# Kernel tuning notes

Hardware: AMD Instinct MI355X
Metric: run time of the kernel (lower is better)

The kernel has to match this reference:

```python
import jax, jax.numpy as jnp
import numpy as np

N_NODES = 100000
N_EDGES = 400000
N_GRAPHS = 4096
F_IN, HID, HEADS, OUT_DIM = 64, 64, 4, 128
NEG_SLOPE = 0.2


def gat_layer(x, src, dst, W, a_s, a_d, b, concat):
    # x: [N, Fin]; W: [Fin, H*C]; a_s/a_d: [H, C]; src/dst: [Etot] (self loops included)
    N = x.shape[0]
    H, C = a_s.shape
    h = (x @ W).reshape(N, H, C)
    e_src = jnp.einsum('nhc,hc->nh', h, a_s)  # [N, H]
    e_dst = jnp.einsum('nhc,hc->nh', h, a_d)
    e = jax.nn.leaky_relu(e_src[src] + e_dst[dst], NEG_SLOPE)  # [Etot, H]
    # segment softmax over edges grouped by destination node
    m = jax.ops.segment_max(e, dst, num_segments=N)
    m = jnp.where(jnp.isfinite(m), m, 0.0)
    ex = jnp.exp(e - m[dst])
    denom = jax.ops.segment_sum(ex, dst, num_segments=N)
    alpha = ex / jnp.maximum(denom[dst], 1e-16)  # [Etot, H]
    out = jax.ops.segment_sum(alpha[:, :, None] * h[src], dst, num_segments=N)  # [N, H, C]
    out = out.reshape(N, H * C) if concat else out.mean(axis=1)
    return out + b


def setup_inputs() -> dict:
    key = jax.random.key(0)
    ks = jax.random.split(key, 32)
    x = jax.random.normal(ks[0], (N_NODES, F_IN), dtype=jnp.float32)
    edge_index = jax.random.randint(ks[1], (2, N_EDGES), 0, N_NODES, dtype=jnp.int64) if jax.config.jax_enable_x64 else jax.random.randint(ks[1], (2, N_EDGES), 0, N_NODES).astype(jnp.int32)
    batch = jnp.sort(jax.random.randint(ks[2], (N_NODES,), 0, N_GRAPHS)).astype(edge_index.dtype)
    s = 0.1
    d = {
        'x': x, 'edge_index': edge_index, 'batch': batch, 'num_graphs': N_GRAPHS,
        'W0': jax.random.normal(ks[3], (F_IN, HEADS * HID), jnp.float32) * s,
        'as0': jax.random.normal(ks[4], (HEADS, HID), jnp.float32) * s,
        'ad0': jax.random.normal(ks[5], (HEADS, HID), jnp.float32) * s,
        'b0': jnp.zeros((HEADS * HID,), jnp.float32),
        'W1': jax.random.normal(ks[6], (HEADS * HID, HEADS * HID), jnp.float32) * s,
        'as1': jax.random.normal(ks[7], (HEADS, HID), jnp.float32) * s,
        'ad1': jax.random.normal(ks[8], (HEADS, HID), jnp.float32) * s,
        'b1': jnp.zeros((HEADS * HID,), jnp.float32),
        'W2': jax.random.normal(ks[9], (HEADS * HID, HEADS * HID), jnp.float32) * s,
        'as2': jax.random.normal(ks[10], (HEADS, HID), jnp.float32) * s,
        'ad2': jax.random.normal(ks[11], (HEADS, HID), jnp.float32) * s,
        'b2': jnp.zeros((HEADS * HID,), jnp.float32),
        'W3': jax.random.normal(ks[12], (HEADS * HID, OUT_DIM), jnp.float32) * s,
        'as3': jax.random.normal(ks[13], (1, OUT_DIM), jnp.float32) * s,
        'ad3': jax.random.normal(ks[14], (1, OUT_DIM), jnp.float32) * s,
        'b3': jnp.zeros((OUT_DIM,), jnp.float32),
        'mW0': jax.random.normal(ks[15], (OUT_DIM, OUT_DIM // 2), jnp.float32) * s,
        'mb0': jnp.zeros((OUT_DIM // 2,), jnp.float32),
        'mW1': jax.random.normal(ks[16], (OUT_DIM // 2, OUT_DIM // 4), jnp.float32) * s,
        'mb1': jnp.zeros((OUT_DIM // 4,), jnp.float32),
        'mW2': jax.random.normal(ks[17], (OUT_DIM // 4, 4), jnp.float32) * s,
        'mb2': jnp.zeros((4,), jnp.float32),
    }
    return d


def reference(x, edge_index, batch, num_graphs, W0, as0, ad0, b0, W1, as1, ad1, b1,
              W2, as2, ad2, b2, W3, as3, ad3, b3, mW0, mb0, mW1, mb1, mW2, mb2):
    N = x.shape[0]
    # PyG GATConv default add_self_loops=True
    loop = jnp.arange(N, dtype=edge_index.dtype)
    src = jnp.concatenate([edge_index[0], loop])
    dst = jnp.concatenate([edge_index[1], loop])
    # dropout layers are identity in eval mode
    h = gat_layer(x, src, dst, W0, as0, ad0, b0, concat=True)
    h = jax.nn.elu(h)
    h = gat_layer(h, src, dst, W1, as1, ad1, b1, concat=True)
    h = jax.nn.elu(h)
    h = gat_layer(h, src, dst, W2, as2, ad2, b2, concat=True)
    h = jax.nn.elu(h)
    h = gat_layer(h, src, dst, W3, as3, ad3, b3, concat=False)  # [N, OUT_DIM]
    # global mean pool per graph
    sums = jax.ops.segment_sum(h, batch, num_segments=num_graphs)
    cnt = jax.ops.segment_sum(jnp.ones((N,), h.dtype), batch, num_segments=num_graphs)
    pooled = sums / jnp.maximum(cnt, 1.0)[:, None]  # [G, OUT_DIM]
    # MLPReadout(out_dim, 4, L=2): 128 -> 64 -> 32 -> 4 with ReLU between
    y = jax.nn.relu(pooled @ mW0 + mb0)
    y = jax.nn.relu(y @ mW1 + mb1)
    y = y @ mW2 + mb2
    return y
```

## Files before the change

kernel.cpp:

```cpp
#include <hip/hip_runtime.h>
#include <math.h>

#define N_NODES 100000
#define N_EDGES 400000
#define N_GRAPHS_C 4096
#define E_TOT (N_EDGES + N_NODES)

static inline int ceil_div(int a, int b) { return (a + b - 1) / b; }

typedef __attribute__((ext_vector_type(8))) short short8v;
typedef __attribute__((ext_vector_type(4))) float float4v;

__device__ __forceinline__ float b2f(unsigned short u) {
  union { unsigned int i; float f; } v;
  v.i = ((unsigned int)u) << 16;
  return v.f;
}
__device__ __forceinline__ unsigned short f2b(float f) {
  union { float f; unsigned int i; } v;
  v.f = f;
  unsigned int x = v.i;
  unsigned int r = x + 0x7fffu + ((x >> 16) & 1u);
  return (unsigned short)(r >> 16);
}


__global__ __launch_bounds__(256) void k_cvt_x(const float* __restrict__ in, unsigned short* __restrict__ out,
                                               int n4) {
  int i = blockIdx.x * 256 + threadIdx.x;
  if (i >= n4) return;
  float4 v = *(const float4*)(in + (size_t)i * 4);
  ushort4 o;
  o.x = f2b(v.x); o.y = f2b(v.y); o.z = f2b(v.z); o.w = f2b(v.w);
  *(ushort4*)(out + (size_t)i * 4) = o;
}

__global__ __launch_bounds__(256) void k_cvt_wt(const float* __restrict__ W, unsigned short* __restrict__ Wt,
                                                int K, int Ncol) {
  int i = blockIdx.x * 256 + threadIdx.x;
  if (i >= K * Ncol) return;
  int n = i / K, k = i % K;
  Wt[(size_t)n * K + k] = f2b(W[(size_t)k * Ncol + n]);
}


__global__ __launch_bounds__(256) void k_count_deg(const int* __restrict__ ei, int* __restrict__ deg) {
  int i = blockIdx.x * 256 + threadIdx.x;
  if (i < N_EDGES) atomicAdd(&deg[ei[N_EDGES + i]], 1);
}

__global__ __launch_bounds__(256) void k_scan(int* __restrict__ deg, int* __restrict__ offs,
                                              int* __restrict__ cursor, int* __restrict__ counter) {
  __shared__ int sm[256];
  __shared__ int sbase;
  int tid = threadIdx.x;
  int n = blockIdx.x * 256 + tid;
  int d = (n < N_NODES) ? (deg[n] + 1) : 0;
  sm[tid] = d;
  __syncthreads();
  for (int off = 1; off < 256; off <<= 1) {
    int v = (tid >= off) ? sm[tid - off] : 0;
    __syncthreads();
    sm[tid] += v;
    __syncthreads();
  }
  if (tid == 255) sbase = atomicAdd(counter, sm[255]);
  __syncthreads();
  int excl = sm[tid] - d;
  if (n < N_NODES) {
    int o = sbase + excl;
    offs[n] = o;
    cursor[n] = o;
    deg[n] = d;
  }
}

__global__ __launch_bounds__(256) void k_scatter(const int* __restrict__ ei, int* __restrict__ cursor,
                                                 int* __restrict__ csr, int* __restrict__ csr_dst) {
  int i = blockIdx.x * 256 + threadIdx.x;
  if (i < N_EDGES) {
    int d = ei[N_EDGES + i];
    int pos = atomicAdd(&cursor[d], 1);
    csr[pos] = ei[i];
    csr_dst[pos] = d;
  } else if (i < E_TOT) {
    int n = i - N_EDGES;
    int pos = atomicAdd(&cursor[n], 1);
    csr[pos] = n;
    csr_dst[pos] = n;
  }
}


__global__ __launch_bounds__(256) void k_gcount(const int* __restrict__ batch, int* __restrict__ gcnt) {
  int i = blockIdx.x * 256 + threadIdx.x;
  if (i < N_NODES) atomicAdd(&gcnt[batch[i]], 1);
}

__global__ __launch_bounds__(256) void k_gscan(const int* __restrict__ gcnt, int* __restrict__ gptr) {
  __shared__ int sm[256];
  __shared__ int srun;
  int tid = threadIdx.x;
  if (tid == 0) srun = 0;
  __syncthreads();
  for (int c = 0; c < N_GRAPHS_C / 256; c++) {
    int idx = c * 256 + tid;
    int v = gcnt[idx];
    sm[tid] = v;
    __syncthreads();
    for (int off = 1; off < 256; off <<= 1) {
      int t = (tid >= off) ? sm[tid - off] : 0;
      __syncthreads();
      sm[tid] += t;
      __syncthreads();
    }
    gptr[idx] = srun + sm[tid] - v;
    __syncthreads();
    if (tid == 0) srun += sm[255];
    __syncthreads();
  }
}


#define LDA 40

template <int ATT>
__global__ __launch_bounds__(256) void k_gemm_bf16(const unsigned short* __restrict__ A,
                                                   const unsigned short* __restrict__ Wt,
                                                   unsigned short* __restrict__ out, int M, int K, int Ncol,
                                                   const float* __restrict__ a_s, const float* __restrict__ a_d,
                                                   float* __restrict__ es, float* __restrict__ ed) {
  __shared__ unsigned short As[128 * LDA];
  __shared__ unsigned short Bs[128 * LDA];
  int tid = threadIdx.x;
  int wave = tid >> 6, lane = tid & 63;
  int quad = lane >> 4, l16 = lane & 15;
  int wrow = (wave & 1) * 64, wcol = (wave >> 1) * 64;
  int row0 = blockIdx.x * 128, col0 = blockIdx.y * 128;

  float4v acc[4][4];
#pragma unroll
  for (int i = 0; i < 4; i++)
#pragma unroll
    for (int j = 0; j < 4; j++) acc[i][j] = (float4v)(0.f);

  int r0 = tid >> 2, c0 = (tid & 3) * 8;
  int r1 = (tid + 256) >> 2, c1 = c0;

  for (int k0 = 0; k0 < K; k0 += 32) {
    uint4 a0 = make_uint4(0, 0, 0, 0), a1 = make_uint4(0, 0, 0, 0);
    if (row0 + r0 < M) a0 = *(const uint4*)(A + (size_t)(row0 + r0) * K + k0 + c0);
    if (row0 + r1 < M) a1 = *(const uint4*)(A + (size_t)(row0 + r1) * K + k0 + c1);
    uint4 b0 = *(const uint4*)(Wt + (size_t)(col0 + r0) * K + k0 + c0);
    uint4 b1 = *(const uint4*)(Wt + (size_t)(col0 + r1) * K + k0 + c1);
    __syncthreads();
    *(uint4*)(&As[r0 * LDA + c0]) = a0;
    *(uint4*)(&As[r1 * LDA + c1]) = a1;
    *(uint4*)(&Bs[r0 * LDA + c0]) = b0;
    *(uint4*)(&Bs[r1 * LDA + c1]) = b1;
    __syncthreads();

    short8v af[4], bf[4];
#pragma unroll
    for (int i = 0; i < 4; i++)
      af[i] = *(const short8v*)(&As[(wrow + i * 16 + l16) * LDA + quad * 8]);
#pragma unroll
    for (int j = 0; j < 4; j++)
      bf[j] = *(const short8v*)(&Bs[(wcol + j * 16 + l16) * LDA + quad * 8]);
#pragma unroll
    for (int i = 0; i < 4; i++)
#pragma unroll
      for (int j = 0; j < 4; j++)
        acc[i][j] = __builtin_amdgcn_mfma_f32_16x16x32_bf16(af[i], bf[j], acc[i][j], 0, 0, 0);
  }

#pragma unroll
  for (int i = 0; i < 4; i++) {
#pragma unroll
    for (int r = 0; r < 4; r++) {
      int m = row0 + wrow + i * 16 + quad * 4 + r;
      if (m < M) {
#pragma unroll
        for (int j = 0; j < 4; j++) {
          int col = col0 + wcol + j * 16 + l16;
          out[(size_t)m * Ncol + col] = f2b(acc[i][j][r]);
        }
      }
    }
  }

  if (ATT) {
    int h = (col0 + wcol) >> 6;
    float as_r[4], ad_r[4];
#pragma unroll
    for (int j = 0; j < 4; j++) {
      as_r[j] = a_s[h * 64 + j * 16 + l16];
      ad_r[j] = a_d[h * 64 + j * 16 + l16];
    }
#pragma unroll
    for (int i = 0; i < 4; i++) {
#pragma unroll
      for (int r = 0; r < 4; r++) {
        float pes = acc[i][0][r] * as_r[0] + acc[i][1][r] * as_r[1] + acc[i][2][r] * as_r[2] + acc[i][3][r] * as_r[3];
        float ped = acc[i][0][r] * ad_r[0] + acc[i][1][r] * ad_r[1] + acc[i][2][r] * ad_r[2] + acc[i][3][r] * ad_r[3];
#pragma unroll
        for (int mk = 1; mk < 16; mk <<= 1) {
          pes += __shfl_xor(pes, mk, 64);
          ped += __shfl_xor(ped, mk, 64);
        }
        if (l16 == 0) {
          int m = row0 + wrow + i * 16 + quad * 4 + r;
          if (m < M) {
            es[m * 4 + h] = pes;
            ed[m * 4 + h] = ped;
          }
        }
      }
    }
  }
}


template <int H, int C>
__global__ __launch_bounds__(256) void k_att(const unsigned short* __restrict__ hbuf,
                                             const float* __restrict__ a_s, const float* __restrict__ a_d,
                                             float* __restrict__ es, float* __restrict__ ed) {
  int idx = blockIdx.x * 256 + threadIdx.x;
  if (idx >= N_NODES * H) return;
  int n = idx / H;
  int h = idx % H;
  const unsigned short* row = hbuf + (size_t)n * (H * C) + h * C;
  const float* asp = a_s + h * C;
  const float* adp = a_d + h * C;
  float s = 0.f, d = 0.f;
#pragma unroll
  for (int c = 0; c < C; c += 8) {
    uint4 u = *(const uint4*)(row + c);
    float4 s0 = *(const float4*)(asp + c);
    float4 s1 = *(const float4*)(asp + c + 4);
    float4 d0 = *(const float4*)(adp + c);
    float4 d1 = *(const float4*)(adp + c + 4);
    float v0 = b2f((unsigned short)(u.x & 0xffff)), v1 = b2f((unsigned short)(u.x >> 16));
    float v2 = b2f((unsigned short)(u.y & 0xffff)), v3 = b2f((unsigned short)(u.y >> 16));
    float v4 = b2f((unsigned short)(u.z & 0xffff)), v5 = b2f((unsigned short)(u.z >> 16));
    float v6 = b2f((unsigned short)(u.w & 0xffff)), v7 = b2f((unsigned short)(u.w >> 16));
    s += v0 * s0.x + v1 * s0.y + v2 * s0.z + v3 * s0.w + v4 * s1.x + v5 * s1.y + v6 * s1.z + v7 * s1.w;
    d += v0 * d0.x + v1 * d0.y + v2 * d0.z + v3 * d0.w + v4 * d1.x + v5 * d1.y + v6 * d1.z + v7 * d1.w;
  }
  es[idx] = s;
  ed[idx] = d;
}


template <int H>
__global__ __launch_bounds__(256) void k_edge_logits(const float* __restrict__ es, const float* __restrict__ ed,
                                                     const int* __restrict__ csr, const int* __restrict__ csr_dst,
                                                     float* __restrict__ ew) {
  int p = blockIdx.x * 256 + threadIdx.x;
  if (p >= E_TOT) return;
  int s = csr[p], d = csr_dst[p];
  if (H == 4) {
    float4 a = *(const float4*)(es + (size_t)s * 4);
    float4 b = *(const float4*)(ed + (size_t)d * 4);
    float4 e;
    e.x = a.x + b.x; e.x = e.x > 0.f ? e.x : 0.2f * e.x;
    e.y = a.y + b.y; e.y = e.y > 0.f ? e.y : 0.2f * e.y;
    e.z = a.z + b.z; e.z = e.z > 0.f ? e.z : 0.2f * e.z;
    e.w = a.w + b.w; e.w = e.w > 0.f ? e.w : 0.2f * e.w;
    *(float4*)(ew + (size_t)p * 4) = e;
  } else {
    float e = es[s] + ed[d];
    ew[p] = e > 0.f ? e : 0.2f * e;
  }
}


template <int H>
__global__ __launch_bounds__(256) void k_stats(float* __restrict__ ew, const int* __restrict__ offs,
                                               const int* __restrict__ deg) {
  int idx = blockIdx.x * 256 + threadIdx.x;
  if (idx >= N_NODES * H) return;
  int n = (H == 1) ? idx : (idx >> 2);
  int h = (H == 1) ? 0 : (idx & 3);
  float* p = ew + (size_t)offs[n] * H + h;
  int c = deg[n];
  float m = -1e30f;
  for (int i = 0; i < c; i++) m = fmaxf(m, p[(size_t)i * H]);
  float s = 0.f;
  for (int i = 0; i < c; i++) s += __expf(p[(size_t)i * H] - m);
  float inv = 1.0f / fmaxf(s, 1e-16f);
  for (int i = 0; i < c; i++) p[(size_t)i * H] = __expf(p[(size_t)i * H] - m) * inv;
}


__device__ __forceinline__ void acc4(float* acc, float w, uint2 u) {
  acc[0] += w * b2f((unsigned short)(u.x & 0xffff));
  acc[1] += w * b2f((unsigned short)(u.x >> 16));
  acc[2] += w * b2f((unsigned short)(u.y & 0xffff));
  acc[3] += w * b2f((unsigned short)(u.y >> 16));
}
__device__ __forceinline__ void acc2(float* acc, float w, unsigned int u) {
  acc[0] += w * b2f((unsigned short)(u & 0xffff));
  acc[1] += w * b2f((unsigned short)(u >> 16));
}

template <int H, int C>
__global__ __launch_bounds__(256) void k_aggregate(const unsigned short* __restrict__ hbuf,
                                                   const float* __restrict__ ew,
                                                   const int* __restrict__ offs, const int* __restrict__ deg,
                                                   const int* __restrict__ csr, const float* __restrict__ bias,
                                                   unsigned short* __restrict__ out, int applyElu) {
  constexpr int F = H * C;
  constexpr int VPL = F / 64;
  int wave = threadIdx.x >> 6;
  int lane = threadIdx.x & 63;
  int n = blockIdx.x * 4 + wave;
  if (n >= N_NODES) return;
  int head = (H == 1) ? 0 : (lane >> 4);
  int start = offs[n];
  int cnt = deg[n];
  const float* ewp = ew + (size_t)start * H + head;
  const int* csrp = csr + start;

  float acc[VPL];
#pragma unroll
  for (int j = 0; j < VPL; j++) acc[j] = 0.f;

  int i = 0;
  for (; i + 4 <= cnt; i += 4) {
    int s0 = csrp[i], s1 = csrp[i + 1], s2 = csrp[i + 2], s3 = csrp[i + 3];
    float w0 = ewp[(size_t)(i + 0) * H];
    float w1 = ewp[(size_t)(i + 1) * H];
    float w2 = ewp[(size_t)(i + 2) * H];
    float w3 = ewp[(size_t)(i + 3) * H];
    if (VPL == 4) {
      uint2 u0 = *(const uint2*)(hbuf + (size_t)s0 * F + lane * 4);
      uint2 u1 = *(const uint2*)(hbuf + (size_t)s1 * F + lane * 4);
      uint2 u2 = *(const uint2*)(hbuf + (size_t)s2 * F + lane * 4);
      uint2 u3 = *(const uint2*)(hbuf + (size_t)s3 * F + lane * 4);
      acc4(acc, w0, u0); acc4(acc, w1, u1); acc4(acc, w2, u2); acc4(acc, w3, u3);
    } else {
      unsigned int u0 = *(const unsigned int*)(hbuf + (size_t)s0 * F + lane * 2);
      unsigned int u1 = *(const unsigned int*)(hbuf + (size_t)s1 * F + lane * 2);
      unsigned int u2 = *(const unsigned int*)(hbuf + (size_t)s2 * F + lane * 2);
      unsigned int u3 = *(const unsigned int*)(hbuf + (size_t)s3 * F + lane * 2);
      acc2(acc, w0, u0); acc2(acc, w1, u1); acc2(acc, w2, u2); acc2(acc, w3, u3);
    }
  }
  for (; i < cnt; i++) {
    int s = csrp[i];
    float w = ewp[(size_t)i * H];
    if (VPL == 4) {
      uint2 u = *(const uint2*)(hbuf + (size_t)s * F + lane * 4);
      acc4(acc, w, u);
    } else {
      unsigned int u = *(const unsigned int*)(hbuf + (size_t)s * F + lane * 2);
      acc2(acc, w, u);
    }
  }

  unsigned short ob[VPL];
#pragma unroll
  for (int j = 0; j < VPL; j++) {
    float v = acc[j] + bias[lane * VPL + j];
    if (applyElu) v = v > 0.f ? v : expm1f(v);
    ob[j] = f2b(v);
  }
  if (VPL == 4) {
    ushort4 o = make_ushort4(ob[0], ob[1], ob[2], ob[3]);
    *(ushort4*)(out + (size_t)n * F + lane * 4) = o;
  } else {
    ushort2 o = make_ushort2(ob[0], ob[1]);
    *(ushort2*)(out + (size_t)n * F + lane * 2) = o;
  }
}


__global__ __launch_bounds__(256) void k_pool_seg(const unsigned short* __restrict__ feat,
                                                  const int* __restrict__ gptr, const int* __restrict__ gcnt,
                                                  float* __restrict__ pool) {
  int wave = threadIdx.x >> 6;
  int lane = threadIdx.x & 63;
  int g = blockIdx.x * 4 + wave;
  if (g >= N_GRAPHS_C) return;
  int start = gptr[g];
  int c = gcnt[g];
  float a0 = 0.f, a1 = 0.f;
  int i = 0;
  for (; i + 2 <= c; i += 2) {
    unsigned int u0 = *(const unsigned int*)(feat + (size_t)(start + i) * 128 + lane * 2);
    unsigned int u1 = *(const unsigned int*)(feat + (size_t)(start + i + 1) * 128 + lane * 2);
    a0 += b2f((unsigned short)(u0 & 0xffff)) + b2f((unsigned short)(u1 & 0xffff));
    a1 += b2f((unsigned short)(u0 >> 16)) + b2f((unsigned short)(u1 >> 16));
  }
  if (i < c) {
    unsigned int u = *(const unsigned int*)(feat + (size_t)(start + i) * 128 + lane * 2);
    a0 += b2f((unsigned short)(u & 0xffff));
    a1 += b2f((unsigned short)(u >> 16));
  }
  float invc = 1.0f / fmaxf((float)c, 1.0f);
  pool[(size_t)g * 128 + lane * 2 + 0] = a0 * invc;
  pool[(size_t)g * 128 + lane * 2 + 1] = a1 * invc;
}


__global__ __launch_bounds__(128) void k_readout(const float* __restrict__ pool,
                                                 const float* __restrict__ mW0, const float* __restrict__ mb0,
                                                 const float* __restrict__ mW1, const float* __restrict__ mb1,
                                                 const float* __restrict__ mW2, const float* __restrict__ mb2,
                                                 float* __restrict__ out) {
  __shared__ float p[128];
  __shared__ float y1[64];
  __shared__ float y2[32];
  int g = blockIdx.x;
  int t = threadIdx.x;
  p[t] = pool[(size_t)g * 128 + t];
  __syncthreads();
  if (t < 64) {
    float a = mb0[t];
#pragma unroll 4
    for (int k = 0; k < 128; k++) a += p[k] * mW0[k * 64 + t];
    y1[t] = a > 0.f ? a : 0.f;
  }
  __syncthreads();
  if (t < 32) {
    float a = mb1[t];
#pragma unroll 4
    for (int k = 0; k < 64; k++) a += y1[k] * mW1[k * 32 + t];
    y2[t] = a > 0.f ? a : 0.f;
  }
  __syncthreads();
  if (t < 4) {
    float a = mb2[t];
#pragma unroll 4
    for (int k = 0; k < 32; k++) a += y2[k] * mW2[k * 4 + t];
    out[(size_t)g * 4 + t] = a;
  }
}


extern "C" void kernel_launch(void* const* d_in, const int* in_sizes, int n_in,
                              void* d_out, int out_size, void* d_ws, size_t ws_size,
                              hipStream_t stream) {
  const float* x = (const float*)d_in[0];
  const int* ei = (const int*)d_in[1];
  const int* batch = (const int*)d_in[2];
  const float* W0 = (const float*)d_in[4];
  const float* as0 = (const float*)d_in[5];
  const float* ad0 = (const float*)d_in[6];
  const float* b0 = (const float*)d_in[7];
  const float* W1 = (const float*)d_in[8];
  const float* as1 = (const float*)d_in[9];
  const float* ad1 = (const float*)d_in[10];
  const float* b1 = (const float*)d_in[11];
  const float* W2 = (const float*)d_in[12];
  const float* as2 = (const float*)d_in[13];
  const float* ad2 = (const float*)d_in[14];
  const float* b2 = (const float*)d_in[15];
  const float* W3 = (const float*)d_in[16];
  const float* as3 = (const float*)d_in[17];
  const float* ad3 = (const float*)d_in[18];
  const float* b3 = (const float*)d_in[19];
  const float* mW0 = (const float*)d_in[20];
  const float* mb0 = (const float*)d_in[21];
  const float* mW1 = (const float*)d_in[22];
  const float* mb1 = (const float*)d_in[23];
  const float* mW2 = (const float*)d_in[24];
  const float* mb2 = (const float*)d_in[25];
  float* out = (float*)d_out;

  char* ws = (char*)d_ws;
  size_t cur = 0;
  auto alloc = [&](size_t bytes) -> char* {
    char* p = ws + cur;
    cur += (bytes + 255) & ~(size_t)255;
    return p;
  };
  unsigned short* featA = (unsigned short*)alloc((size_t)N_NODES * 256 * 2);
  unsigned short* hB = (unsigned short*)alloc((size_t)N_NODES * 256 * 2);
  unsigned short* xb = (unsigned short*)alloc((size_t)N_NODES * 64 * 2);
  unsigned short* wt0 = (unsigned short*)alloc((size_t)256 * 64 * 2);
  unsigned short* wt1 = (unsigned short*)alloc((size_t)256 * 256 * 2);
  unsigned short* wt2 = (unsigned short*)alloc((size_t)256 * 256 * 2);
  unsigned short* wt3 = (unsigned short*)alloc((size_t)128 * 256 * 2);
  float* es = (float*)alloc((size_t)N_NODES * 4 * sizeof(float));
  float* ed = (float*)alloc((size_t)N_NODES * 4 * sizeof(float));
  float* ew = (float*)alloc((size_t)E_TOT * 4 * sizeof(float));
  int* deg = (int*)alloc((size_t)N_NODES * sizeof(int));
  int* offs = (int*)alloc((size_t)N_NODES * sizeof(int));
  int* cursor = (int*)alloc((size_t)N_NODES * sizeof(int));
  int* csr = (int*)alloc((size_t)E_TOT * sizeof(int));
  int* csr_dst = (int*)alloc((size_t)E_TOT * sizeof(int));
  float* pool = (float*)alloc((size_t)N_GRAPHS_C * 128 * sizeof(float));
  int* gcnt = (int*)alloc((size_t)N_GRAPHS_C * sizeof(int));
  int* gptr = (int*)alloc((size_t)N_GRAPHS_C * sizeof(int));
  int* counter = (int*)alloc(256);
  (void)ws_size; (void)in_sizes; (void)n_in; (void)out_size;

  k_cvt_x<<<ceil_div(N_NODES * 64 / 4, 256), 256, 0, stream>>>(x, xb, N_NODES * 64 / 4);
  k_cvt_wt<<<ceil_div(64 * 256, 256), 256, 0, stream>>>(W0, wt0, 64, 256);
  k_cvt_wt<<<ceil_div(256 * 256, 256), 256, 0, stream>>>(W1, wt1, 256, 256);
  k_cvt_wt<<<ceil_div(256 * 256, 256), 256, 0, stream>>>(W2, wt2, 256, 256);
  k_cvt_wt<<<ceil_div(256 * 128, 256), 256, 0, stream>>>(W3, wt3, 256, 128);

  hipMemsetAsync(deg, 0, (size_t)N_NODES * sizeof(int), stream);
  hipMemsetAsync(counter, 0, sizeof(int), stream);
  hipMemsetAsync(gcnt, 0, (size_t)N_GRAPHS_C * sizeof(int), stream);
  k_count_deg<<<ceil_div(N_EDGES, 256), 256, 0, stream>>>(ei, deg);
  k_scan<<<ceil_div(N_NODES, 256), 256, 0, stream>>>(deg, offs, cursor, counter);
  k_scatter<<<ceil_div(E_TOT, 256), 256, 0, stream>>>(ei, cursor, csr, csr_dst);
  k_gcount<<<ceil_div(N_NODES, 256), 256, 0, stream>>>(batch, gcnt);
  k_gscan<<<1, 256, 0, stream>>>(gcnt, gptr);

  int gm = ceil_div(N_NODES, 128);
  dim3 g256(gm, 2), g128(gm, 1);
  int aggBlocks = ceil_div(N_NODES, 4);
  int edgeBlocks = ceil_div(E_TOT, 256);
  int statBlocks4 = ceil_div(N_NODES * 4, 256);
  int statBlocks1 = ceil_div(N_NODES, 256);

  k_gemm_bf16<1><<<g256, 256, 0, stream>>>(xb, wt0, hB, N_NODES, 64, 256, as0, ad0, es, ed);
  k_edge_logits<4><<<edgeBlocks, 256, 0, stream>>>(es, ed, csr, csr_dst, ew);
  k_stats<4><<<statBlocks4, 256, 0, stream>>>(ew, offs, deg);
  k_aggregate<4, 64><<<aggBlocks, 256, 0, stream>>>(hB, ew, offs, deg, csr, b0, featA, 1);

  k_gemm_bf16<1><<<g256, 256, 0, stream>>>(featA, wt1, hB, N_NODES, 256, 256, as1, ad1, es, ed);
  k_edge_logits<4><<<edgeBlocks, 256, 0, stream>>>(es, ed, csr, csr_dst, ew);
  k_stats<4><<<statBlocks4, 256, 0, stream>>>(ew, offs, deg);
  k_aggregate<4, 64><<<aggBlocks, 256, 0, stream>>>(hB, ew, offs, deg, csr, b1, featA, 1);

  k_gemm_bf16<1><<<g256, 256, 0, stream>>>(featA, wt2, hB, N_NODES, 256, 256, as2, ad2, es, ed);
  k_edge_logits<4><<<edgeBlocks, 256, 0, stream>>>(es, ed, csr, csr_dst, ew);
  k_stats<4><<<statBlocks4, 256, 0, stream>>>(ew, offs, deg);
  k_aggregate<4, 64><<<aggBlocks, 256, 0, stream>>>(hB, ew, offs, deg, csr, b2, featA, 1);

  k_gemm_bf16<0><<<g128, 256, 0, stream>>>(featA, wt3, hB, N_NODES, 256, 128, nullptr, nullptr, nullptr, nullptr);
  k_att<1, 128><<<statBlocks1, 256, 0, stream>>>(hB, as3, ad3, es, ed);
  k_edge_logits<1><<<edgeBlocks, 256, 0, stream>>>(es, ed, csr, csr_dst, ew);
  k_stats<1><<<statBlocks1, 256, 0, stream>>>(ew, offs, deg);
  k_aggregate<1, 128><<<aggBlocks, 256, 0, stream>>>(hB, ew, offs, deg, csr, b3, featA, 0);

  k_pool_seg<<<ceil_div(N_GRAPHS_C, 4), 256, 0, stream>>>(featA, gptr, gcnt, pool);
  k_readout<<<N_GRAPHS_C, 128, 0, stream>>>(pool, mW0, mb0, mW1, mb1, mW2, mb2, out);
}
```

Measured before the change: 676.0 us.

## Fuse setup, logits/softmax, last-layer attention and pool/readout kernels to cut launches

Merges the four weight conversions into one launch and the degree and graph counts into one launch, and clears the counters with a single memset over a contiguous range. Folds the per-edge logit kernel into the segment-softmax stats kernel, which drops the csr_dst array. Moves the last layer's attention dot products into the GEMM epilogue through a shared-memory reduction, and fuses mean pooling into the readout MLP. This removes many launches and intermediate buffers, but the fused logits kernel now gathers es per destination thread serially, and pooling runs one thread per feature.

Result: faster. 656.3 us (-2.9%).

```diff
diff --git a/kernel.cpp b/kernel.cpp
--- a/kernel.cpp
+++ b/kernel.cpp
@@ -35,18 +35,30 @@
   *(ushort4*)(out + (size_t)i * 4) = o;
 }
 
-__global__ __launch_bounds__(256) void k_cvt_wt(const float* __restrict__ W, unsigned short* __restrict__ Wt,
-                                                int K, int Ncol) {
+__device__ __forceinline__ void cvt_one(const float* __restrict__ W, unsigned short* __restrict__ Wt,
+                                        int K, int Ncol, int idx) {
+  int n = idx / K, k = idx % K;
+  Wt[(size_t)n * K + k] = f2b(W[(size_t)k * Ncol + n]);
+}
+
+__global__ __launch_bounds__(256) void k_cvt_w_all(const float* __restrict__ W0, unsigned short* __restrict__ wt0,
+                                                   const float* __restrict__ W1, unsigned short* __restrict__ wt1,
+                                                   const float* __restrict__ W2, unsigned short* __restrict__ wt2,
+                                                   const float* __restrict__ W3, unsigned short* __restrict__ wt3) {
   int i = blockIdx.x * 256 + threadIdx.x;
-  if (i >= K * Ncol) return;
-  int n = i / K, k = i % K;
-  Wt[(size_t)n * K + k] = f2b(W[(size_t)k * Ncol + n]);
-}
-
-
-__global__ __launch_bounds__(256) void k_count_deg(const int* __restrict__ ei, int* __restrict__ deg) {
+  const int s0 = 64 * 256, s1 = s0 + 256 * 256, s2 = s1 + 256 * 256, s3 = s2 + 256 * 128;
+  if (i < s0) cvt_one(W0, wt0, 64, 256, i);
+  else if (i < s1) cvt_one(W1, wt1, 256, 256, i - s0);
+  else if (i < s2) cvt_one(W2, wt2, 256, 256, i - s1);
+  else if (i < s3) cvt_one(W3, wt3, 256, 128, i - s2);
+}
+
+
+__global__ __launch_bounds__(256) void k_count_deg_g(const int* __restrict__ ei, int* __restrict__ deg,
+                                                     const int* __restrict__ batch, int* __restrict__ gcnt) {
   int i = blockIdx.x * 256 + threadIdx.x;
   if (i < N_EDGES) atomicAdd(&deg[ei[N_EDGES + i]], 1);
+  if (i < N_NODES) atomicAdd(&gcnt[batch[i]], 1);
 }
 
 __global__ __launch_bounds__(256) void k_scan(int* __restrict__ deg, int* __restrict__ offs,
@@ -76,25 +88,17 @@
 }
 
 __global__ __launch_bounds__(256) void k_scatter(const int* __restrict__ ei, int* __restrict__ cursor,
-                                                 int* __restrict__ csr, int* __restrict__ csr_dst) {
+                                                 int* __restrict__ csr) {
   int i = blockIdx.x * 256 + threadIdx.x;
   if (i < N_EDGES) {
     int d = ei[N_EDGES + i];
     int pos = atomicAdd(&cursor[d], 1);
     csr[pos] = ei[i];
-    csr_dst[pos] = d;
   } else if (i < E_TOT) {
     int n = i - N_EDGES;
     int pos = atomicAdd(&cursor[n], 1);
     csr[pos] = n;
-    csr_dst[pos] = n;
-  }
-}
-
-
-__global__ __launch_bounds__(256) void k_gcount(const int* __restrict__ batch, int* __restrict__ gcnt) {
-  int i = blockIdx.x * 256 + threadIdx.x;
-  if (i < N_NODES) atomicAdd(&gcnt[batch[i]], 1);
+  }
 }
 
 __global__ __launch_bounds__(256) void k_gscan(const int* __restrict__ gcnt, int* __restrict__ gptr) {
@@ -189,7 +193,7 @@
     }
   }
 
-  if (ATT) {
+  if (ATT == 1) {
     int h = (col0 + wcol) >> 6;
     float as_r[4], ad_r[4];
 #pragma unroll
@@ -218,77 +222,70 @@
       }
     }
   }
-}
-
-
-template <int H, int C>
-__global__ __launch_bounds__(256) void k_att(const unsigned short* __restrict__ hbuf,
-                                             const float* __restrict__ a_s, const float* __restrict__ a_d,
-                                             float* __restrict__ es, float* __restrict__ ed) {
-  int idx = blockIdx.x * 256 + threadIdx.x;
-  if (idx >= N_NODES * H) return;
-  int n = idx / H;
-  int h = idx % H;
-  const unsigned short* row = hbuf + (size_t)n * (H * C) + h * C;
-  const float* asp = a_s + h * C;
-  const float* adp = a_d + h * C;
-  float s = 0.f, d = 0.f;
-#pragma unroll
-  for (int c = 0; c < C; c += 8) {
-    uint4 u = *(const uint4*)(row + c);
-    float4 s0 = *(const float4*)(asp + c);
-    float4 s1 = *(const float4*)(asp + c + 4);
-    float4 d0 = *(const float4*)(adp + c);
-    float4 d1 = *(const float4*)(adp + c + 4);
-    float v0 = b2f((unsigned short)(u.x & 0xffff)), v1 = b2f((unsigned short)(u.x >> 16));
-    float v2 = b2f((unsigned short)(u.y & 0xffff)), v3 = b2f((unsigned short)(u.y >> 16));
-    float v4 = b2f((unsigned short)(u.z & 0xffff)), v5 = b2f((unsigned short)(u.z >> 16));
-    float v6 = b2f((unsigned short)(u.w & 0xffff)), v7 = b2f((unsigned short)(u.w >> 16));
-    s += v0 * s0.x + v1 * s0.y + v2 * s0.z + v3 * s0.w + v4 * s1.x + v5 * s1.y + v6 * s1.z + v7 * s1.w;
-    d += v0 * d0.x + v1 * d0.y + v2 * d0.z + v3 * d0.w + v4 * d1.x + v5 * d1.y + v6 * d1.z + v7 * d1.w;
-  }
-  es[idx] = s;
-  ed[idx] = d;
+
+  if (ATT == 2) {
+    __shared__ float ps[128][2], pd[128][2];
+    float as_r[4], ad_r[4];
+#pragma unroll
+    for (int j = 0; j < 4; j++) {
+      as_r[j] = a_s[wcol + j * 16 + l16];
+      ad_r[j] = a_d[wcol + j * 16 + l16];
+    }
+#pragma unroll
+    for (int i = 0; i < 4; i++) {
+#pragma unroll
+      for (int r = 0; r < 4; r++) {
+        float pes = acc[i][0][r] * as_r[0] + acc[i][1][r] * as_r[1] + acc[i][2][r] * as_r[2] + acc[i][3][r] * as_r[3];
+        float ped = acc[i][0][r] * ad_r[0] + acc[i][1][r] * ad_r[1] + acc[i][2][r] * ad_r[2] + acc[i][3][r] * ad_r[3];
+#pragma unroll
+        for (int mk = 1; mk < 16; mk <<= 1) {
+          pes += __shfl_xor(pes, mk, 64);
+          ped += __shfl_xor(ped, mk, 64);
+        }
+        if (l16 == 0) {
+          int lr = wrow + i * 16 + quad * 4 + r;
+          ps[lr][wcol >> 6] = pes;
+          pd[lr][wcol >> 6] = ped;
+        }
+      }
+    }
+    __syncthreads();
+    if (tid < 128) {
+      int m = row0 + tid;
+      if (m < M) {
+        es[m] = ps[tid][0] + ps[tid][1];
+        ed[m] = pd[tid][0] + pd[tid][1];
+      }
+    }
+  }
 }
 
 
 template <int H>
-__global__ __launch_bounds__(256) void k_edge_logits(const float* __restrict__ es, const float* __restrict__ ed,
-                                                     const int* __restrict__ csr, const int* __restrict__ csr_dst,
-                                                     float* __restrict__ ew) {
-  int p = blockIdx.x * 256 + threadIdx.x;
-  if (p >= E_TOT) return;
-  int s = csr[p], d = csr_dst[p];
-  if (H == 4) {
-    float4 a = *(const float4*)(es + (size_t)s * 4);
-    float4 b = *(const float4*)(ed + (size_t)d * 4);
-    float4 e;
-    e.x = a.x + b.x; e.x = e.x > 0.f ? e.x : 0.2f * e.x;
-    e.y = a.y + b.y; e.y = e.y > 0.f ? e.y : 0.2f * e.y;
-    e.z = a.z + b.z; e.z = e.z > 0.f ? e.z : 0.2f * e.z;
-    e.w = a.w + b.w; e.w = e.w > 0.f ? e.w : 0.2f * e.w;
-    *(float4*)(ew + (size_t)p * 4) = e;
-  } else {
-    float e = es[s] + ed[d];
-    ew[p] = e > 0.f ? e : 0.2f * e;
-  }
-}
-
-
-template <int H>
-__global__ __launch_bounds__(256) void k_stats(float* __restrict__ ew, const int* __restrict__ offs,
-                                               const int* __restrict__ deg) {
+__global__ __launch_bounds__(256) void k_logits_stats(const float* __restrict__ es, const float* __restrict__ ed,
+                                                      const int* __restrict__ csr, const int* __restrict__ offs,
+                                                      const int* __restrict__ deg, float* __restrict__ ew) {
   int idx = blockIdx.x * 256 + threadIdx.x;
   if (idx >= N_NODES * H) return;
   int n = (H == 1) ? idx : (idx >> 2);
   int h = (H == 1) ? 0 : (idx & 3);
-  float* p = ew + (size_t)offs[n] * H + h;
+  int start = offs[n];
   int c = deg[n];
+  const int* csrp = csr + start;
+  float* p = ew + (size_t)start * H + h;
+  float edn = ed[n * H + h];
+
   float m = -1e30f;
-  for (int i = 0; i < c; i++) m = fmaxf(m, p[(size_t)i * H]);
-  float s = 0.f;
-  for (int i = 0; i < c; i++) s += __expf(p[(size_t)i * H] - m);
-  float inv = 1.0f / fmaxf(s, 1e-16f);
+  for (int i = 0; i < c; i++) {
+    int s = csrp[i];
+    float e = es[s * H + h] + edn;
+    e = e > 0.f ? e : 0.2f * e;
+    p[(size_t)i * H] = e;
+    m = fmaxf(m, e);
+  }
+  float sum = 0.f;
+  for (int i = 0; i < c; i++) sum += __expf(p[(size_t)i * H] - m);
+  float inv = 1.0f / fmaxf(sum, 1e-16f);
   for (int i = 0; i < c; i++) p[(size_t)i * H] = __expf(p[(size_t)i * H] - m) * inv;
 }
 
@@ -376,65 +373,42 @@
 }
 
 
-__global__ __launch_bounds__(256) void k_pool_seg(const unsigned short* __restrict__ feat,
-                                                  const int* __restrict__ gptr, const int* __restrict__ gcnt,
-                                                  float* __restrict__ pool) {
-  int wave = threadIdx.x >> 6;
-  int lane = threadIdx.x & 63;
-  int g = blockIdx.x * 4 + wave;
-  if (g >= N_GRAPHS_C) return;
-  int start = gptr[g];
-  int c = gcnt[g];
-  float a0 = 0.f, a1 = 0.f;
-  int i = 0;
-  for (; i + 2 <= c; i += 2) {
-    unsigned int u0 = *(const unsigned int*)(feat + (size_t)(start + i) * 128 + lane * 2);
-    unsigned int u1 = *(const unsigned int*)(feat + (size_t)(start + i + 1) * 128 + lane * 2);
-    a0 += b2f((unsigned short)(u0 & 0xffff)) + b2f((unsigned short)(u1 & 0xffff));
-    a1 += b2f((unsigned short)(u0 >> 16)) + b2f((unsigned short)(u1 >> 16));
-  }
-  if (i < c) {
-    unsigned int u = *(const unsigned int*)(feat + (size_t)(start + i) * 128 + lane * 2);
-    a0 += b2f((unsigned short)(u & 0xffff));
-    a1 += b2f((unsigned short)(u >> 16));
-  }
-  float invc = 1.0f / fmaxf((float)c, 1.0f);
-  pool[(size_t)g * 128 + lane * 2 + 0] = a0 * invc;
-  pool[(size_t)g * 128 + lane * 2 + 1] = a1 * invc;
-}
-
-
-__global__ __launch_bounds__(128) void k_readout(const float* __restrict__ pool,
-                                                 const float* __restrict__ mW0, const float* __restrict__ mb0,
-                                                 const float* __restrict__ mW1, const float* __restrict__ mb1,
-                                                 const float* __restrict__ mW2, const float* __restrict__ mb2,
-                                                 float* __restrict__ out) {
+__global__ __launch_bounds__(128) void k_pool_readout(const unsigned short* __restrict__ feat,
+                                                      const int* __restrict__ gptr, const int* __restrict__ gcnt,
+                                                      const float* __restrict__ mW0, const float* __restrict__ mb0,
+                                                      const float* __restrict__ mW1, const float* __restrict__ mb1,
+                                                      const float* __restrict__ mW2, const float* __restrict__ mb2,
+                                                      float* __restrict__ out) {
   __shared__ float p[128];
   __shared__ float y1[64];
   __shared__ float y2[32];
   int g = blockIdx.x;
   int t = threadIdx.x;
-  p[t] = pool[(size_t)g * 128 + t];
+  int start = gptr[g];
+  int c = gcnt[g];
+  float a = 0.f;
+  for (int i = 0; i < c; i++) a += b2f(feat[(size_t)(start + i) * 128 + t]);
+  p[t] = a / fmaxf((float)c, 1.0f);
   __syncthreads();
   if (t < 64) {
-    float a = mb0[t];
+    float v = mb0[t];
 #pragma unroll 4
-    for (int k = 0; k < 128; k++) a += p[k] * mW0[k * 64 + t];
-    y1[t] = a > 0.f ? a : 0.f;
+    for (int k = 0; k < 128; k++) v += p[k] * mW0[k * 64 + t];
+    y1[t] = v > 0.f ? v : 0.f;
   }
   __syncthreads();
   if (t < 32) {
-    float a = mb1[t];
+    float v = mb1[t];
 #pragma unroll 4
-    for (int k = 0; k < 64; k++) a += y1[k] * mW1[k * 32 + t];
-    y2[t] = a > 0.f ? a : 0.f;
+    for (int k = 0; k < 64; k++) v += y1[k] * mW1[k * 32 + t];
+    y2[t] = v > 0.f ? v : 0.f;
   }
   __syncthreads();
   if (t < 4) {
-    float a = mb2[t];
+    float v = mb2[t];
 #pragma unroll 4
-    for (int k = 0; k < 32; k++) a += y2[k] * mW2[k * 4 + t];
-    out[(size_t)g * 4 + t] = a;
+    for (int k = 0; k < 32; k++) v += y2[k] * mW2[k * 4 + t];
+    out[(size_t)g * 4 + t] = v;
   }
 }
 
@@ -487,59 +461,45 @@
   float* ed = (float*)alloc((size_t)N_NODES * 4 * sizeof(float));
   float* ew = (float*)alloc((size_t)E_TOT * 4 * sizeof(float));
   int* deg = (int*)alloc((size_t)N_NODES * sizeof(int));
+  int* counter = (int*)alloc(256);
+  int* gcnt = (int*)alloc((size_t)N_GRAPHS_C * sizeof(int));
+  size_t zeroBytes = (char*)(gcnt + N_GRAPHS_C) - (char*)deg;
   int* offs = (int*)alloc((size_t)N_NODES * sizeof(int));
   int* cursor = (int*)alloc((size_t)N_NODES * sizeof(int));
   int* csr = (int*)alloc((size_t)E_TOT * sizeof(int));
-  int* csr_dst = (int*)alloc((size_t)E_TOT * sizeof(int));
-  float* pool = (float*)alloc((size_t)N_GRAPHS_C * 128 * sizeof(float));
-  int* gcnt = (int*)alloc((size_t)N_GRAPHS_C * sizeof(int));
   int* gptr = (int*)alloc((size_t)N_GRAPHS_C * sizeof(int));
-  int* counter = (int*)alloc(256);
   (void)ws_size; (void)in_sizes; (void)n_in; (void)out_size;
 
   k_cvt_x<<<ceil_div(N_NODES * 64 / 4, 256), 256, 0, stream>>>(x, xb, N_NODES * 64 / 4);
-  k_cvt_wt<<<ceil_div(64 * 256, 256), 256, 0, stream>>>(W0, wt0, 64, 256);
-  k_cvt_wt<<<ceil_div(256 * 256, 256), 256, 0, stream>>>(W1, wt1, 256, 256);
-  k_cvt_wt<<<ceil_div(256 * 256, 256), 256, 0, stream>>>(W2, wt2, 256, 256);
-  k_cvt_wt<<<ceil_div(256 * 128, 256), 256, 0, stream>>>(W3, wt3, 256, 128);
-
-  hipMemsetAsync(deg, 0, (size_t)N_NODES * sizeof(int), stream);
-  hipMemsetAsync(counter, 0, sizeof(int), stream);
-  hipMemsetAsync(gcnt, 0, (size_t)N_GRAPHS_C * sizeof(int), stream);
-  k_count_deg<<<ceil_div(N_EDGES, 256), 256, 0, stream>>>(ei, deg);
+  k_cvt_w_all<<<ceil_div(64 * 256 + 2 * 256 * 256 + 256 * 128, 256), 256, 0, stream>>>(W0, wt0, W1, wt1, W2, wt2, W3, wt3);
+
+  hipMemsetAsync(deg, 0, zeroBytes, stream);
+  k_count_deg_g<<<ceil_div(N_EDGES, 256), 256, 0, stream>>>(ei, deg, batch, gcnt);
   k_scan<<<ceil_div(N_NODES, 256), 256, 0, stream>>>(deg, offs, cursor, counter);
-  k_scatter<<<ceil_div(E_TOT, 256), 256, 0, stream>>>(ei, cursor, csr, csr_dst);
-  k_gcount<<<ceil_div(N_NODES, 256), 256, 0, stream>>>(batch, gcnt);
+  k_scatter<<<ceil_div(E_TOT, 256), 256, 0, stream>>>(ei, cursor, csr);
   k_gscan<<<1, 256, 0, stream>>>(gcnt, gptr);
 
   int gm = ceil_div(N_NODES, 128);
   dim3 g256(gm, 2), g128(gm, 1);
   int aggBlocks = ceil_div(N_NODES, 4);
-  int edgeBlocks = ceil_div(E_TOT, 256);
-  int statBlocks4 = ceil_div(N_NODES * 4, 256);
-  int statBlocks1 = ceil_div(N_NODES, 256);
+  int lsBlocks4 = ceil_div(N_NODES * 4, 256);
+  int lsBlocks1 = ceil_div(N_NODES, 256);
 
   k_gemm_bf16<1><<<g256, 256, 0, stream>>>(xb, wt0, hB, N_NODES, 64, 256, as0, ad0, es, ed);
-  k_edge_logits<4><<<edgeBlocks, 256, 0, stream>>>(es, ed, csr, csr_dst, ew);
-  k_stats<4><<<statBlocks4, 256, 0, stream>>>(ew, offs, deg);
+  k_logits_stats<4><<<lsBlocks4, 256, 0, stream>>>(es, ed, csr, offs, deg, ew);
   k_aggregate<4, 64><<<aggBlocks, 256, 0, stream>>>(hB, ew, offs, deg, csr, b0, featA, 1);
 
   k_gemm_bf16<1><<<g256, 256, 0, stream>>>(featA, wt1, hB, N_NODES, 256, 256, as1, ad1, es, ed);
-  k_edge_logits<4><<<edgeBlocks, 256, 0, stream>>>(es, ed, csr, csr_dst, ew);
-  k_stats<4><<<statBlocks4, 256, 0, stream>>>(ew, offs, deg);
+  k_logits_stats<4><<<lsBlocks4, 256, 0, stream>>>(es, ed, csr, offs, deg, ew);
   k_aggregate<4, 64><<<aggBlocks, 256, 0, stream>>>(hB, ew, offs, deg, csr, b1, featA, 1);
 
   k_gemm_bf16<1><<<g256, 256, 0, stream>>>(featA, wt2, hB, N_NODES, 256, 256, as2, ad2, es, ed);
-  k_edge_logits<4><<<edgeBlocks, 256, 0, stream>>>(es, ed, csr, csr_dst, ew);
-  k_stats<4><<<statBlocks4, 256, 0, stream>>>(ew, offs, deg);
+  k_logits_stats<4><<<lsBlocks4, 256, 0, stream>>>(es, ed, csr, offs, deg, ew);
   k_aggregate<4, 64><<<aggBlocks, 256, 0, stream>>>(hB, ew, offs, deg, csr, b2, featA, 1);
 
-  k_gemm_bf16<0><<<g128, 256, 0, stream>>>(featA, wt3, hB, N_NODES, 256, 128, nullptr, nullptr, nullptr, nullptr);
-  k_att<1, 128><<<statBlocks1, 256, 0, stream>>>(hB, as3, ad3, es, ed);
-  k_edge_logits<1><<<edgeBlocks, 256, 0, stream>>>(es, ed, csr, csr_dst, ew);
-  k_stats<1><<<statBlocks1, 256, 0, stream>>>(ew, offs, deg);
+  k_gemm_bf16<2><<<g128, 256, 0, stream>>>(featA, wt3, hB, N_NODES, 256, 128, as3, ad3, es, ed);
+  k_logits_stats<1><<<lsBlocks1, 256, 0, stream>>>(es, ed, csr, offs, deg, ew);
   k_aggregate<1, 128><<<aggBlocks, 256, 0, stream>>>(hB, ew, offs, deg, csr, b3, featA, 0);
 
-  k_pool_seg<<<ceil_div(N_GRAPHS_C, 4), 256, 0, stream>>>(featA, gptr, gcnt, pool);
-  k_readout<<<N_GRAPHS_C, 128, 0, stream>>>(pool, mW0, mb0, mW1, mb1, mW2, mb2, out);
-}
+  k_pool_readout<<<N_GRAPHS_C, 128, 0, stream>>>(featA, gptr, gcnt, mW0, mb0, mW1, mb1, mW2, mb2, out);
+}
```
